# Kernel tuning notes

Measured on AMD Instinct MI355X. Metric: run time of the kernel, lower is better.

Reference implementation:

```python
import jax, jax.numpy as jnp
import numpy as np

N_IN, N_HID, N_OUT = 200, 256, 2
BN_EPS = 1e-5


def _mlp(x, W1, b1, W2, b2):
    # two-layer MLP with ELU activations (dropout prob = 0.0 -> omitted)
    h = jax.nn.elu(x @ W1 + b1)
    return jax.nn.elu(h @ W2 + b2)


def _batch_norm(x, gamma, beta):
    # torch BatchNorm1d in training mode over flattened (B*E) rows, biased variance
    m = x.mean(axis=(0, 1))
    v = x.var(axis=(0, 1))
    return (x - m) * jax.lax.rsqrt(v + BN_EPS) * gamma + beta


def setup_inputs() -> dict:
    key = jax.random.key(0)
    ks = jax.random.split(key, 12)
    B, N, T, D = 32, 100, 50, 4
    inputs = jax.random.normal(ks[0], (B, N, T, D), dtype=jnp.float32)
    # one-hot receiver/sender matrices over all N*(N-1) ordered off-diagonal pairs
    idx = np.array([(i, j) for i in range(N) for j in range(N) if i != j])
    eye = np.eye(N, dtype=np.float32)
    rel_rec = jnp.asarray(eye[idx[:, 0]])   # [E, N]
    rel_send = jnp.asarray(eye[idx[:, 1]])  # [E, N]

    def lin(k, fi, fo):  # xavier_normal weight
        std = float(np.sqrt(2.0 / (fi + fo)))
        return jax.random.normal(k, (fi, fo), dtype=jnp.float32) * std

    b = lambda n: jnp.full((n,), 0.1, dtype=jnp.float32)
    return dict(
        inputs=inputs, rel_rec=rel_rec, rel_send=rel_send,
        mlp1_W1=lin(ks[1], N_IN, N_HID), mlp1_b1=b(N_HID),
        mlp1_W2=lin(ks[2], N_HID, N_HID), mlp1_b2=b(N_HID),
        mlp2_W1=lin(ks[3], 2 * N_HID, N_HID), mlp2_b1=b(N_HID),
        mlp2_W2=lin(ks[4], N_HID, N_HID), mlp2_b2=b(N_HID),
        mlp3_W1=lin(ks[5], N_HID, N_HID), mlp3_b1=b(N_HID),
        mlp3_W2=lin(ks[6], N_HID, N_HID), mlp3_b2=b(N_HID),
        mlp4_W1=lin(ks[7], 3 * N_HID, N_HID), mlp4_b1=b(N_HID),
        mlp4_W2=lin(ks[8], N_HID, N_HID), mlp4_b2=b(N_HID),
        mlp4_bn_gamma=jnp.ones((N_HID,), jnp.float32),
        mlp4_bn_beta=jnp.zeros((N_HID,), jnp.float32),
        fc_W=lin(ks[9], N_HID, N_OUT), fc_b=b(N_OUT),
    )


def reference(inputs, rel_rec, rel_send,
              mlp1_W1, mlp1_b1, mlp1_W2, mlp1_b2,
              mlp2_W1, mlp2_b1, mlp2_W2, mlp2_b2,
              mlp3_W1, mlp3_b1, mlp3_W2, mlp3_b2,
              mlp4_W1, mlp4_b1, mlp4_W2, mlp4_b2,
              mlp4_bn_gamma, mlp4_bn_beta, fc_W, fc_b):
    B, N = inputs.shape[0], inputs.shape[1]
    x = inputs.reshape(B, N, -1)                       # [B, N, T*D]
    x = _mlp(x, mlp1_W1, mlp1_b1, mlp1_W2, mlp1_b2)     # [B, N, H]

    def node2edge(h):
        recv = jnp.einsum('en,bnh->beh', rel_rec, h)
        send = jnp.einsum('en,bnh->beh', rel_send, h)
        return jnp.concatenate([send, recv], axis=2)    # [B, E, 2H]

    x = node2edge(x)
    x = _mlp(x, mlp2_W1, mlp2_b1, mlp2_W2, mlp2_b2)     # [B, E, H]
    x_skip = x
    # factor=True branch
    incoming = jnp.einsum('en,beh->bnh', rel_rec, x) / x.shape[1]  # edge2node, /N per code
    x = _mlp(incoming, mlp3_W1, mlp3_b1, mlp3_W2, mlp3_b2)
    x = node2edge(x)                                    # [B, E, 2H]
    x = jnp.concatenate([x, x_skip], axis=2)            # [B, E, 3H]
    x = _mlp(x, mlp4_W1, mlp4_b1, mlp4_W2, mlp4_b2)
    x = _batch_norm(x, mlp4_bn_gamma, mlp4_bn_beta)
    return x @ fc_W + fc_b                              # [B, E, n_out]
```

## Files before the change

kernel.cpp:

```cpp
#include <hip/hip_runtime.h>
#include <math.h>


typedef unsigned short ushort_t;
typedef __bf16 bf16x8 __attribute__((ext_vector_type(8)));
typedef float  f32x4  __attribute__((ext_vector_type(4)));

#define E_EDGES 9900
#define NNODE   100
#define HID     256
#define M_BIG   316800
#define M_SMALL 3200
#define NBLK2   (M_BIG / 128)

__device__ __forceinline__ float bf2f(ushort_t u) {
    union { unsigned int i; float f; } v; v.i = ((unsigned int)u) << 16; return v.f;
}
__device__ __forceinline__ ushort_t f2bf(float f) {
    union { float f; unsigned int i; } v; v.f = f;
    return (ushort_t)((v.i + 0x7fffu + ((v.i >> 16) & 1u)) >> 16);
}
__device__ __forceinline__ float elu_f(float x) {
    return x > 0.f ? x : (__expf(x) - 1.f);
}

__global__ __launch_bounds__(256)
void wcvt_all(const float* __restrict__ s0, const float* __restrict__ s1,
              const float* __restrict__ s2, const float* __restrict__ s3,
              const float* __restrict__ s4, const float* __restrict__ s5,
              const float* __restrict__ s6, const float* __restrict__ s7,
              ushort_t* d0, ushort_t* d1, ushort_t* d2, ushort_t* d3,
              ushort_t* d4, ushort_t* d5, ushort_t* d6, ushort_t* d7)
{
    int bid = blockIdx.x;
    const float* S; ushort_t* D; int Kd, Kr, t;
    if      (bid < 16)  { S = s0; D = d0; Kd = 256; Kr = 200; t = bid; }
    else if (bid < 32)  { S = s1; D = d1; Kd = 256; Kr = 256; t = bid - 16; }
    else if (bid < 64)  { S = s2; D = d2; Kd = 512; Kr = 512; t = bid - 32; }
    else if (bid < 80)  { S = s3; D = d3; Kd = 256; Kr = 256; t = bid - 64; }
    else if (bid < 96)  { S = s4; D = d4; Kd = 256; Kr = 256; t = bid - 80; }
    else if (bid < 112) { S = s5; D = d5; Kd = 256; Kr = 256; t = bid - 96; }
    else if (bid < 160) { S = s6; D = d6; Kd = 768; Kr = 768; t = bid - 112; }
    else                { S = s7; D = d7; Kd = 256; Kr = 256; t = bid - 160; }
    int k0 = (t >> 2) * 64, c0 = (t & 3) * 64;
    __shared__ float Sh[64][65];
    int tid = threadIdx.x;
    #pragma unroll
    for (int i = 0; i < 16; ++i) {
        int idx = tid + i * 256;
        int kk = idx >> 6, cc = idx & 63;
        Sh[kk][cc] = (k0 + kk < Kr) ? S[(size_t)(k0 + kk) * 256 + c0 + cc] : 0.f;
    }
    __syncthreads();
    int col = tid & 63;
    int kb  = (tid >> 6) * 16;
    ushort_t* dst = D + (size_t)(c0 + col) * Kd + k0 + kb;
    #pragma unroll
    for (int jj = 0; jj < 4; ++jj) {
        ushort4 u;
        u.x = f2bf(Sh[kb + 4 * jj + 0][col]);
        u.y = f2bf(Sh[kb + 4 * jj + 1][col]);
        u.z = f2bf(Sh[kb + 4 * jj + 2][col]);
        u.w = f2bf(Sh[kb + 4 * jj + 3][col]);
        *(ushort4*)(dst + 4 * jj) = u;
    }
}

__device__ __forceinline__ void gemm32(const ushort_t S[32][264],
                                       const ushort_t* __restrict__ WT,
                                       int wstr, int kcn,
                                       int w, int ln15, int klane,
                                       f32x4 acc[2][4])
{
    #pragma unroll
    for (int r = 0; r < 2; ++r)
        #pragma unroll
        for (int c = 0; c < 4; ++c)
            acc[r][c][0] = acc[r][c][1] = acc[r][c][2] = acc[r][c][3] = 0.f;
    int wch[4];
    #pragma unroll
    for (int c = 0; c < 4; ++c) wch[c] = (w * 64 + 16 * c + ln15) * wstr;
    bf16x8 wf0[4];
    #pragma unroll
    for (int c = 0; c < 4; ++c)
        wf0[c] = *(const bf16x8*)(WT + wch[c] + klane);
    for (int kc = 0; kc < kcn; ++kc) {
        bf16x8 wf1[4];
        if (kc + 1 < kcn) {
            #pragma unroll
            for (int c = 0; c < 4; ++c)
                wf1[c] = *(const bf16x8*)(WT + wch[c] + (kc + 1) * 32 + klane);
        }
        bf16x8 af[2];
        #pragma unroll
        for (int r = 0; r < 2; ++r)
            af[r] = *(const bf16x8*)&S[16 * r + ln15][kc * 32 + klane];
        #pragma unroll
        for (int r = 0; r < 2; ++r)
            #pragma unroll
            for (int c = 0; c < 4; ++c)
                acc[r][c] = __builtin_amdgcn_mfma_f32_16x16x32_bf16(wf0[c], af[r], acc[r][c], 0, 0, 0);
        #pragma unroll
        for (int c = 0; c < 4; ++c) wf0[c] = wf1[c];
    }
}

__device__ __forceinline__ void park32(ushort_t D[32][264], f32x4 acc[2][4],
                                       const float* __restrict__ bias,
                                       int act, int w, int ln15, int q)
{
    #pragma unroll
    for (int c = 0; c < 4; ++c) {
        float4 bv = bias ? *(const float4*)&bias[w * 64 + 16 * c + 4 * q]
                         : make_float4(0.f, 0.f, 0.f, 0.f);
        #pragma unroll
        for (int r = 0; r < 2; ++r) {
            float o0 = acc[r][c][0] + bv.x;
            float o1 = acc[r][c][1] + bv.y;
            float o2 = acc[r][c][2] + bv.z;
            float o3 = acc[r][c][3] + bv.w;
            if (act) { o0 = elu_f(o0); o1 = elu_f(o1); o2 = elu_f(o2); o3 = elu_f(o3); }
            ushort4 u;
            u.x = f2bf(o0); u.y = f2bf(o1); u.z = f2bf(o2); u.w = f2bf(o3);
            *(ushort4*)&D[16 * r + ln15][w * 64 + 16 * c + 4 * q] = u;
        }
    }
}

__global__ __launch_bounds__(256, 4)
void mlp_pq(const float* __restrict__ Xf, int Kreal, int kcN, float xscale,
            const ushort_t* __restrict__ W1T, const float* __restrict__ b1,
            const ushort_t* __restrict__ W2T, const float* __restrict__ b2,
            const ushort_t* __restrict__ WPT, int wsPQ,
            const float* __restrict__ bP, ushort_t* __restrict__ Pout,
            const ushort_t* __restrict__ WQT, ushort_t* __restrict__ Qout)
{
    __shared__ ushort_t Abuf[32][264];
    __shared__ ushort_t Bbuf[32][264];
    const int tid = threadIdx.x;
    const int w = tid >> 6;
    const int l = tid & 63;
    const int ln15 = l & 15;
    const int q = l >> 4;
    const int klane = 8 * q;
    const int Rbase = blockIdx.x * 32;

    {
        int row = tid >> 3, seg = tid & 7;
        if (seg < kcN) {
            ushort_t tmp[32];
            const float* src = Xf + (size_t)(Rbase + row) * Kreal + seg * 32;
            #pragma unroll
            for (int u = 0; u < 32; ++u)
                tmp[u] = (seg * 32 + u < Kreal) ? f2bf(src[u] * xscale) : (ushort_t)0;
            #pragma unroll
            for (int u = 0; u < 4; ++u)
                *(uint4*)&Abuf[row][seg * 32 + u * 8] = *(uint4*)&tmp[u * 8];
        }
    }
    __syncthreads();

    f32x4 acc[2][4];
    gemm32(Abuf, W1T, 256, kcN, w, ln15, klane, acc);
    park32(Bbuf, acc, b1, 1, w, ln15, q);
    __syncthreads();
    gemm32(Bbuf, W2T, 256, 8, w, ln15, klane, acc);
    park32(Abuf, acc, b2, 1, w, ln15, q);
    __syncthreads();
    gemm32(Abuf, WPT, wsPQ, 8, w, ln15, klane, acc);
    park32(Bbuf, acc, bP, 0, w, ln15, q);
    __syncthreads();
    f32x4 acq[2][4];
    gemm32(Abuf, WQT, wsPQ, 8, w, ln15, klane, acq);
    #pragma unroll
    for (int m = 0; m < 4; ++m) {
        int ch = tid + m * 256;
        int row = ch >> 5;
        int o = (ch & 31) * 8;
        *(uint4*)&Pout[(size_t)(Rbase + row) * 256 + o] = *(const uint4*)&Bbuf[row][o];
    }
    __syncthreads();
    park32(Bbuf, acq, nullptr, 0, w, ln15, q);
    __syncthreads();
    #pragma unroll
    for (int m = 0; m < 4; ++m) {
        int ch = tid + m * 256;
        int row = ch >> 5;
        int o = (ch & 31) * 8;
        *(uint4*)&Qout[(size_t)(Rbase + row) * 256 + o] = *(const uint4*)&Bbuf[row][o];
    }
}

__global__ __launch_bounds__(256, 2)
void edge_mlp2(const ushort_t* __restrict__ Pb, const ushort_t* __restrict__ Qb,
               const ushort_t* __restrict__ W2T,
               const float* __restrict__ b2,
               ushort_t* __restrict__ Y, float* __restrict__ aux)
{
    __shared__ ushort_t As[128][264];
    const int tid = threadIdx.x;
    const int w = tid >> 6;
    const int l = tid & 63;
    const int ln15 = l & 15;
    const int q = l >> 4;
    const int klane = 8 * q;
    const int Rbase = blockIdx.x * 128;

    for (int h = 0; h < 2; ++h) {
        int row = (tid >> 2) + 64 * h;
        int R = Rbase + row;
        int b = R / E_EDGES;
        int e = R - b * E_EDGES;
        int i = e / 99;
        int k = e - 99 * i;
        int j = k + (k >= i ? 1 : 0);
        const ushort_t* prow = Pb + (size_t)(b * NNODE + j) * HID;
        const ushort_t* qrow = Qb + (size_t)(b * NNODE + i) * HID;
        int off = (tid & 3) * 8;
        uint4 pv[8], qv[8];
        #pragma unroll
        for (int u = 0; u < 8; ++u) {
            int o = off + u * 32;
            pv[u] = *(const uint4*)(prow + o);
            qv[u] = *(const uint4*)(qrow + o);
        }
        #pragma unroll
        for (int u = 0; u < 8; ++u) {
            int o = off + u * 32;
            union { uint4 v; ushort_t s[8]; } pu, qu, hu;
            pu.v = pv[u]; qu.v = qv[u];
            #pragma unroll
            for (int x = 0; x < 8; ++x)
                hu.s[x] = f2bf(elu_f(bf2f(pu.s[x]) + bf2f(qu.s[x])));
            *(uint4*)&As[row][o] = hu.v;
        }
    }
    __syncthreads();

    f32x4 acc[8][4];
    #pragma unroll
    for (int r = 0; r < 8; ++r)
        #pragma unroll
        for (int c = 0; c < 4; ++c)
            acc[r][c][0] = acc[r][c][1] = acc[r][c][2] = acc[r][c][3] = 0.f;
    int wch[4];
    #pragma unroll
    for (int c = 0; c < 4; ++c) wch[c] = (w * 64 + 16 * c + ln15) * 256;
    {
        bf16x8 wf0[4];
        #pragma unroll
        for (int c = 0; c < 4; ++c)
            wf0[c] = *(const bf16x8*)(W2T + wch[c] + klane);
        #pragma unroll
        for (int kc = 0; kc < 8; ++kc) {
            bf16x8 wf1[4];
            if (kc < 7) {
                #pragma unroll
                for (int c = 0; c < 4; ++c)
                    wf1[c] = *(const bf16x8*)(W2T + wch[c] + (kc + 1) * 32 + klane);
            }
            bf16x8 af[8];
            #pragma unroll
            for (int r = 0; r < 8; ++r)
                af[r] = *(const bf16x8*)&As[16 * r + ln15][kc * 32 + klane];
            #pragma unroll
            for (int r = 0; r < 8; ++r)
                #pragma unroll
                for (int c = 0; c < 4; ++c)
                    acc[r][c] = __builtin_amdgcn_mfma_f32_16x16x32_bf16(wf0[c], af[r], acc[r][c], 0, 0, 0);
            #pragma unroll
            for (int c = 0; c < 4; ++c) wf0[c] = wf1[c];
        }
    }
    __syncthreads();

    #pragma unroll
    for (int c = 0; c < 4; ++c) {
        float4 bv = *(const float4*)&b2[w * 64 + 16 * c + 4 * q];
        #pragma unroll
        for (int r = 0; r < 8; ++r) {
            ushort4 u;
            u.x = f2bf(elu_f(acc[r][c][0] + bv.x));
            u.y = f2bf(elu_f(acc[r][c][1] + bv.y));
            u.z = f2bf(elu_f(acc[r][c][2] + bv.z));
            u.w = f2bf(elu_f(acc[r][c][3] + bv.w));
            *(ushort4*)&As[16 * r + ln15][w * 64 + 16 * c + 4 * q] = u;
        }
    }
    __syncthreads();

    #pragma unroll
    for (int m = 0; m < 16; ++m) {
        int ch = tid + m * 256;
        int row = ch >> 5;
        int o = (ch & 31) * 8;
        *(uint4*)&Y[((size_t)(Rbase + row)) * 256 + o] = *(const uint4*)&As[row][o];
    }

    if (tid < 64) {
        int c4 = tid * 4;
        int bn = Rbase / 99;
        int left = 99 - (Rbase - bn * 99);
        float s[4] = {0.f, 0.f, 0.f, 0.f};
        for (int r = 0; r < 128; ++r) {
            union { ushort4 v; ushort_t e[4]; } u;
            u.v = *(const ushort4*)&As[r][c4];
            #pragma unroll
            for (int g = 0; g < 4; ++g) s[g] += bf2f(u.e[g]);
            if (--left == 0) {
                #pragma unroll
                for (int g = 0; g < 4; ++g) {
                    atomicAdd(&aux[(size_t)bn * 256 + c4 + g], s[g]);
                    s[g] = 0.f;
                }
                ++bn; left = 99;
            }
        }
        #pragma unroll
        for (int g = 0; g < 4; ++g)
            atomicAdd(&aux[(size_t)bn * 256 + c4 + g], s[g]);
    }
}

__global__ __launch_bounds__(256, 2)
void edge_mlp4(const ushort_t* __restrict__ Pb, const ushort_t* __restrict__ Qb,
               const ushort_t* __restrict__ X2,
               const ushort_t* __restrict__ WaT, int wsA,
               const ushort_t* __restrict__ WbT, int wsB,
               const float* __restrict__ b2,
               ushort_t* __restrict__ Y, ushort_t* __restrict__ pstat)
{
    __shared__ ushort_t As[128][264];
    const int tid = threadIdx.x;
    const int w = tid >> 6;
    const int l = tid & 63;
    const int ln15 = l & 15;
    const int q = l >> 4;
    const int klane = 8 * q;
    const int Rbase = blockIdx.x * 128;

    uint4 xv[2][8];
    #pragma unroll
    for (int h = 0; h < 2; ++h) {
        int row = (tid >> 2) + 64 * h;
        const ushort_t* xrow = X2 + (size_t)(Rbase + row) * 256;
        int off = (tid & 3) * 8;
        #pragma unroll
        for (int u = 0; u < 8; ++u) xv[h][u] = *(const uint4*)(xrow + off + u * 32);
    }

    int oP[8], oQ[8];
    #pragma unroll
    for (int r = 0; r < 8; ++r) {
        int R = Rbase + 16 * r + ln15;
        int b = R / E_EDGES;
        int e = R - b * E_EDGES;
        int i = e / 99;
        int k = e - 99 * i;
        int j = k + (k >= i ? 1 : 0);
        oP[r] = (b * NNODE + j) * HID;
        oQ[r] = (b * NNODE + i) * HID;
    }
    ushort4 pv0[8], qv0[8];
    {
        int ch0 = w * 64 + 4 * q;
        #pragma unroll
        for (int r = 0; r < 8; ++r) {
            pv0[r] = *(const ushort4*)(Pb + oP[r] + ch0);
            qv0[r] = *(const ushort4*)(Qb + oQ[r] + ch0);
        }
    }

    #pragma unroll
    for (int h = 0; h < 2; ++h) {
        int row = (tid >> 2) + 64 * h;
        int off = (tid & 3) * 8;
        #pragma unroll
        for (int u = 0; u < 8; ++u) *(uint4*)&As[row][off + u * 32] = xv[h][u];
    }
    __syncthreads();

    f32x4 acc[8][4];
    int wchA[4], wchB[4];
    #pragma unroll
    for (int c = 0; c < 4; ++c) {
        wchA[c] = (w * 64 + 16 * c + ln15) * wsA;
        wchB[c] = (w * 64 + 16 * c + ln15) * wsB;
    }

    #pragma unroll
    for (int r = 0; r < 8; ++r)
        #pragma unroll
        for (int c = 0; c < 4; ++c)
            acc[r][c][0] = acc[r][c][1] = acc[r][c][2] = acc[r][c][3] = 0.f;
    {
        bf16x8 wf0[4];
        #pragma unroll
        for (int c = 0; c < 4; ++c)
            wf0[c] = *(const bf16x8*)(WaT + wchA[c] + klane);
        #pragma unroll
        for (int kc = 0; kc < 8; ++kc) {
            bf16x8 wf1[4];
            if (kc < 7) {
                #pragma unroll
                for (int c = 0; c < 4; ++c)
                    wf1[c] = *(const bf16x8*)(WaT + wchA[c] + (kc + 1) * 32 + klane);
            }
            bf16x8 af[8];
            #pragma unroll
            for (int r = 0; r < 8; ++r)
                af[r] = *(const bf16x8*)&As[16 * r + ln15][kc * 32 + klane];
            #pragma unroll
            for (int r = 0; r < 8; ++r)
                #pragma unroll
                for (int c = 0; c < 4; ++c)
                    acc[r][c] = __builtin_amdgcn_mfma_f32_16x16x32_bf16(wf0[c], af[r], acc[r][c], 0, 0, 0);
            #pragma unroll
            for (int c = 0; c < 4; ++c) wf0[c] = wf1[c];
        }
    }
    __syncthreads();

    #pragma unroll
    for (int c = 0; c < 4; ++c) {
        ushort4 pv1[8], qv1[8];
        if (c < 3) {
            int chn = w * 64 + 16 * (c + 1) + 4 * q;
            #pragma unroll
            for (int r = 0; r < 8; ++r) {
                pv1[r] = *(const ushort4*)(Pb + oP[r] + chn);
                qv1[r] = *(const ushort4*)(Qb + oQ[r] + chn);
            }
        }
        int ch = w * 64 + 16 * c + 4 * q;
        #pragma unroll
        for (int r = 0; r < 8; ++r) {
            union { ushort4 v; ushort_t s[4]; } pu, qu;
            pu.v = pv0[r]; qu.v = qv0[r];
            ushort4 u;
            u.x = f2bf(elu_f(acc[r][c][0] + bf2f(pu.s[0]) + bf2f(qu.s[0])));
            u.y = f2bf(elu_f(acc[r][c][1] + bf2f(pu.s[1]) + bf2f(qu.s[1])));
            u.z = f2bf(elu_f(acc[r][c][2] + bf2f(pu.s[2]) + bf2f(qu.s[2])));
            u.w = f2bf(elu_f(acc[r][c][3] + bf2f(pu.s[3]) + bf2f(qu.s[3])));
            *(ushort4*)&As[16 * r + ln15][ch] = u;
        }
        #pragma unroll
        for (int r = 0; r < 8; ++r) { pv0[r] = pv1[r]; qv0[r] = qv1[r]; }
    }
    __syncthreads();

    #pragma unroll
    for (int r = 0; r < 8; ++r)
        #pragma unroll
        for (int c = 0; c < 4; ++c)
            acc[r][c][0] = acc[r][c][1] = acc[r][c][2] = acc[r][c][3] = 0.f;
    {
        bf16x8 wf0[4];
        #pragma unroll
        for (int c = 0; c < 4; ++c)
            wf0[c] = *(const bf16x8*)(WbT + wchB[c] + klane);
        #pragma unroll
        for (int kc = 0; kc < 8; ++kc) {
            bf16x8 wf1[4];
            if (kc < 7) {
                #pragma unroll
                for (int c = 0; c < 4; ++c)
                    wf1[c] = *(const bf16x8*)(WbT + wchB[c] + (kc + 1) * 32 + klane);
            }
            bf16x8 af[8];
            #pragma unroll
            for (int r = 0; r < 8; ++r)
                af[r] = *(const bf16x8*)&As[16 * r + ln15][kc * 32 + klane];
            #pragma unroll
            for (int r = 0; r < 8; ++r)
                #pragma unroll
                for (int c = 0; c < 4; ++c)
                    acc[r][c] = __builtin_amdgcn_mfma_f32_16x16x32_bf16(wf0[c], af[r], acc[r][c], 0, 0, 0);
            #pragma unroll
            for (int c = 0; c < 4; ++c) wf0[c] = wf1[c];
        }
    }
    __syncthreads();

    #pragma unroll
    for (int c = 0; c < 4; ++c) {
        float4 bv = *(const float4*)&b2[w * 64 + 16 * c + 4 * q];
        #pragma unroll
        for (int r = 0; r < 8; ++r) {
            ushort4 u;
            u.x = f2bf(elu_f(acc[r][c][0] + bv.x));
            u.y = f2bf(elu_f(acc[r][c][1] + bv.y));
            u.z = f2bf(elu_f(acc[r][c][2] + bv.z));
            u.w = f2bf(elu_f(acc[r][c][3] + bv.w));
            *(ushort4*)&As[16 * r + ln15][w * 64 + 16 * c + 4 * q] = u;
        }
    }
    __syncthreads();

    #pragma unroll
    for (int m = 0; m < 16; ++m) {
        int ch = tid + m * 256;
        int row = ch >> 5;
        int o = (ch & 31) * 8;
        *(uint4*)&Y[((size_t)(Rbase + row)) * 256 + o] = *(const uint4*)&As[row][o];
    }

    if (tid < 64) {
        int c4 = tid * 4;
        float s[4] = {0.f, 0.f, 0.f, 0.f};
        float qq[4] = {0.f, 0.f, 0.f, 0.f};
        for (int r = 0; r < 128; ++r) {
            union { ushort4 v; ushort_t e[4]; } u;
            u.v = *(const ushort4*)&As[r][c4];
            #pragma unroll
            for (int g = 0; g < 4; ++g) {
                float v = bf2f(u.e[g]);
                s[g] += v;
                qq[g] = fmaf(v, v, qq[g]);
            }
        }
        size_t base = (size_t)blockIdx.x * 512;
        ushort4 us, uq;
        us.x = f2bf(s[0]);  us.y = f2bf(s[1]);  us.z = f2bf(s[2]);  us.w = f2bf(s[3]);
        uq.x = f2bf(qq[0]); uq.y = f2bf(qq[1]); uq.z = f2bf(qq[2]); uq.w = f2bf(qq[3]);
        *(ushort4*)&pstat[base + c4]       = us;
        *(ushort4*)&pstat[base + 256 + c4] = uq;
    }
}

__global__ __launch_bounds__(256)
void reduce_stats(const ushort_t* __restrict__ pstat, float* __restrict__ stats)
{
    int c = threadIdx.x;
    float s = 0.f, q = 0.f;
    for (int b = blockIdx.x; b < NBLK2; b += 64) {
        size_t base = (size_t)b * 512;
        s += bf2f(pstat[base + c]);
        q += bf2f(pstat[base + 256 + c]);
    }
    atomicAdd(&stats[c], s);
    atomicAdd(&stats[256 + c], q);
}

__global__ __launch_bounds__(256)
void fold_kernel(const float* __restrict__ stats,
                 const float* __restrict__ gamma, const float* __restrict__ beta,
                 const float* __restrict__ fcW, const float* __restrict__ fcb,
                 float* __restrict__ fold)
{
    __shared__ float red0[256], red1[256];
    int c = threadIdx.x;
    float mean  = stats[c] * (1.f / M_BIG);
    float var   = stats[256 + c] * (1.f / M_BIG) - mean * mean;
    float inv   = rsqrtf(var + 1e-5f);
    float scale = inv * gamma[c];
    float sh    = beta[c] - mean * scale;
    float w0 = fcW[c * 2 + 0], w1 = fcW[c * 2 + 1];
    fold[c * 2 + 0] = scale * w0;
    fold[c * 2 + 1] = scale * w1;
    red0[c] = sh * w0;
    red1[c] = sh * w1;
    __syncthreads();
    for (int off = 128; off > 0; off >>= 1) {
        if (c < off) { red0[c] += red0[c + off]; red1[c] += red1[c + off]; }
        __syncthreads();
    }
    if (c == 0) {
        fold[512] = red0[0] + fcb[0];
        fold[513] = red1[0] + fcb[1];
    }
}

__global__ __launch_bounds__(256)
void final_kernel(const ushort_t* __restrict__ x4, const float* __restrict__ fold,
                  float* __restrict__ out)
{
    int tid  = threadIdx.x;
    int l32  = tid & 31;
    int g    = tid >> 5;
    int R = blockIdx.x * 8 + g;
    int c0 = l32 * 8;
    union { uint4 qv; ushort_t s[8]; } u;
    u.qv = *(const uint4*)(x4 + (size_t)R * 256 + c0);
    float a0 = 0.f, a1 = 0.f;
    #pragma unroll
    for (int j = 0; j < 8; ++j) {
        float v = bf2f(u.s[j]);
        a0 = fmaf(v, fold[(c0 + j) * 2 + 0], a0);
        a1 = fmaf(v, fold[(c0 + j) * 2 + 1], a1);
    }
    #pragma unroll
    for (int off = 16; off > 0; off >>= 1) {
        a0 += __shfl_down(a0, off);
        a1 += __shfl_down(a1, off);
    }
    if (l32 == 0) {
        out[(size_t)R * 2 + 0] = a0 + fold[512];
        out[(size_t)R * 2 + 1] = a1 + fold[513];
    }
}

extern "C" void kernel_launch(void* const* d_in, const int* in_sizes, int n_in,
                              void* d_out, int out_size, void* d_ws, size_t ws_size,
                              hipStream_t stream)
{
    (void)in_sizes; (void)n_in; (void)out_size; (void)ws_size;

    const float* inputs = (const float*)d_in[0];
    const float* m1W1 = (const float*)d_in[3];
    const float* m1b1 = (const float*)d_in[4];
    const float* m1W2 = (const float*)d_in[5];
    const float* m1b2 = (const float*)d_in[6];
    const float* m2W1 = (const float*)d_in[7];
    const float* m2b1 = (const float*)d_in[8];
    const float* m2W2 = (const float*)d_in[9];
    const float* m2b2 = (const float*)d_in[10];
    const float* m3W1 = (const float*)d_in[11];
    const float* m3b1 = (const float*)d_in[12];
    const float* m3W2 = (const float*)d_in[13];
    const float* m3b2 = (const float*)d_in[14];
    const float* m4W1 = (const float*)d_in[15];
    const float* m4b1 = (const float*)d_in[16];
    const float* m4W2 = (const float*)d_in[17];
    const float* m4b2 = (const float*)d_in[18];
    const float* gamma = (const float*)d_in[19];
    const float* beta  = (const float*)d_in[20];
    const float* fcW   = (const float*)d_in[21];
    const float* fcb   = (const float*)d_in[22];
    float* out = (float*)d_out;

    char* ws = (char*)d_ws;
    const size_t BIGB = (size_t)M_BIG * 256 * 2;
    const size_t HB   = (size_t)M_SMALL * 256 * 2;
    const size_t SM4  = (size_t)M_SMALL * 256 * 4;
    ushort_t* bigX     = (ushort_t*)ws;
    ushort_t* pstat    = (ushort_t*)(ws + BIGB);
    float*    incoming = (float*)(ws + BIGB + 2 * HB);
    ushort_t* Pbuf     = (ushort_t*)(ws + BIGB + 2 * HB + SM4);
    ushort_t* Qbuf     = (ushort_t*)(ws + BIGB + 3 * HB + SM4);
    float*    stats    = (float*)(ws + BIGB + 4 * HB + SM4);
    float*    fold     = stats + 512;
    ushort_t* w1t      = (ushort_t*)(ws + BIGB + 4 * HB + SM4 + 8192);
    ushort_t* w1bt     = w1t  + 256 * 256;
    ushort_t* w2pt     = w1bt + 256 * 256;
    ushort_t* w2t      = w2pt + 256 * 512;
    ushort_t* w3at     = w2t  + 256 * 256;
    ushort_t* w3bt     = w3at + 256 * 256;
    ushort_t* w4pt     = w3bt + 256 * 256;
    ushort_t* w4bt     = w4pt + 256 * 768;

    hipMemsetAsync(stats, 0, 2048, stream);
    hipMemsetAsync(incoming, 0, SM4, stream);

    dim3 blk(256);
    wcvt_all<<<176, blk, 0, stream>>>(m1W1, m1W2, m2W1, m2W2, m3W1, m3W2, m4W1, m4W2,
                                      w1t, w1bt, w2pt, w2t, w3at, w3bt, w4pt, w4bt);
    mlp_pq<<<100, blk, 0, stream>>>(inputs, 200, 7, 1.f,
                                    w1t, m1b1, w1bt, m1b2,
                                    w2pt, 512, m2b1, Pbuf,
                                    w2pt + 256, Qbuf);
    edge_mlp2<<<NBLK2, blk, 0, stream>>>(Pbuf, Qbuf, w2t, m2b2, bigX, incoming);
    mlp_pq<<<100, blk, 0, stream>>>(incoming, 256, 8, 1.f / 9900.f,
                                    w3at, m3b1, w3bt, m3b2,
                                    w4pt, 768, m4b1, Pbuf,
                                    w4pt + 256, Qbuf);
    edge_mlp4<<<NBLK2, blk, 0, stream>>>(Pbuf, Qbuf, bigX,
                                         w4pt + 512, 768, w4bt, 256,
                                         m4b2, bigX, pstat);
    reduce_stats<<<64, blk, 0, stream>>>(pstat, stats);
    fold_kernel<<<1, blk, 0, stream>>>(stats, gamma, beta, fcW, fcb, fold);
    final_kernel<<<M_BIG / 8, blk, 0, stream>>>(bigX, fold, out);
}
```

Measured before the change: 520.1 us.

## Use 512-thread blocks in edge MLP kernels with 32-column warp tiles

The edge_mlp2 and edge_mlp4 kernels move from 256 to 512 threads per block. Each of the eight warps now owns 32 output columns instead of 64, which halves the accumulator registers and allows more waves per CU. The GEMM loop is moved into a shared helper that issues A-fragment loads in two groups of four rows to reduce register pressure. In edge_mlp4 the software prefetch of P/Q rows is removed, trading some latency hiding for lower register use, and each warp now does more LDS reads per MFMA.

Result: faster. 494.5 us (-4.9%).

```diff
diff --git a/kernel.cpp b/kernel.cpp
--- a/kernel.cpp
+++ b/kernel.cpp
@@ -191,7 +191,49 @@
     }
 }
 
-__global__ __launch_bounds__(256, 2)
+__device__ __forceinline__ void gemm128cs(const ushort_t As[128][264],
+                                          const ushort_t* __restrict__ WT,
+                                          int wstr, int w, int ln15, int klane,
+                                          f32x4 acc[8][2])
+{
+    #pragma unroll
+    for (int r = 0; r < 8; ++r)
+        #pragma unroll
+        for (int c = 0; c < 2; ++c)
+            acc[r][c][0] = acc[r][c][1] = acc[r][c][2] = acc[r][c][3] = 0.f;
+    int wch[2];
+    #pragma unroll
+    for (int c = 0; c < 2; ++c) wch[c] = (w * 32 + 16 * c + ln15) * wstr;
+    bf16x8 wf0[2];
+    #pragma unroll
+    for (int c = 0; c < 2; ++c)
+        wf0[c] = *(const bf16x8*)(WT + wch[c] + klane);
+    #pragma unroll
+    for (int kc = 0; kc < 8; ++kc) {
+        bf16x8 wf1[2];
+        if (kc < 7) {
+            #pragma unroll
+            for (int c = 0; c < 2; ++c)
+                wf1[c] = *(const bf16x8*)(WT + wch[c] + (kc + 1) * 32 + klane);
+        }
+        #pragma unroll
+        for (int g = 0; g < 2; ++g) {
+            bf16x8 af[4];
+            #pragma unroll
+            for (int r = 0; r < 4; ++r)
+                af[r] = *(const bf16x8*)&As[16 * (4 * g + r) + ln15][kc * 32 + klane];
+            #pragma unroll
+            for (int r = 0; r < 4; ++r)
+                #pragma unroll
+                for (int c = 0; c < 2; ++c)
+                    acc[4 * g + r][c] = __builtin_amdgcn_mfma_f32_16x16x32_bf16(wf0[c], af[r], acc[4 * g + r][c], 0, 0, 0);
+        }
+        #pragma unroll
+        for (int c = 0; c < 2; ++c) wf0[c] = wf1[c];
+    }
+}
+
+__global__ __launch_bounds__(512, 4)
 void edge_mlp2(const ushort_t* __restrict__ Pb, const ushort_t* __restrict__ Qb,
                const ushort_t* __restrict__ W2T,
                const float* __restrict__ b2,
@@ -206,8 +248,8 @@
     const int klane = 8 * q;
     const int Rbase = blockIdx.x * 128;
 
-    for (int h = 0; h < 2; ++h) {
-        int row = (tid >> 2) + 64 * h;
+    {
+        int row = tid >> 2;
         int R = Rbase + row;
         int b = R / E_EDGES;
         int e = R - b * E_EDGES;
@@ -237,46 +279,13 @@
     }
     __syncthreads();
 
-    f32x4 acc[8][4];
-    #pragma unroll
-    for (int r = 0; r < 8; ++r)
-        #pragma unroll
-        for (int c = 0; c < 4; ++c)
-            acc[r][c][0] = acc[r][c][1] = acc[r][c][2] = acc[r][c][3] = 0.f;
-    int wch[4];
-    #pragma unroll
-    for (int c = 0; c < 4; ++c) wch[c] = (w * 64 + 16 * c + ln15) * 256;
-    {
-        bf16x8 wf0[4];
-        #pragma unroll
-        for (int c = 0; c < 4; ++c)
-            wf0[c] = *(const bf16x8*)(W2T + wch[c] + klane);
-        #pragma unroll
-        for (int kc = 0; kc < 8; ++kc) {
-            bf16x8 wf1[4];
-            if (kc < 7) {
-                #pragma unroll
-                for (int c = 0; c < 4; ++c)
-                    wf1[c] = *(const bf16x8*)(W2T + wch[c] + (kc + 1) * 32 + klane);
-            }
-            bf16x8 af[8];
-            #pragma unroll
-            for (int r = 0; r < 8; ++r)
-                af[r] = *(const bf16x8*)&As[16 * r + ln15][kc * 32 + klane];
-            #pragma unroll
-            for (int r = 0; r < 8; ++r)
-                #pragma unroll
-                for (int c = 0; c < 4; ++c)
-                    acc[r][c] = __builtin_amdgcn_mfma_f32_16x16x32_bf16(wf0[c], af[r], acc[r][c], 0, 0, 0);
-            #pragma unroll
-            for (int c = 0; c < 4; ++c) wf0[c] = wf1[c];
-        }
-    }
-    __syncthreads();
-
-    #pragma unroll
-    for (int c = 0; c < 4; ++c) {
-        float4 bv = *(const float4*)&b2[w * 64 + 16 * c + 4 * q];
+    f32x4 acc[8][2];
+    gemm128cs(As, W2T, 256, w, ln15, klane, acc);
+    __syncthreads();
+
+    #pragma unroll
+    for (int c = 0; c < 2; ++c) {
+        float4 bv = *(const float4*)&b2[w * 32 + 16 * c + 4 * q];
         #pragma unroll
         for (int r = 0; r < 8; ++r) {
             ushort4 u;
@@ -284,14 +293,14 @@
             u.y = f2bf(elu_f(acc[r][c][1] + bv.y));
             u.z = f2bf(elu_f(acc[r][c][2] + bv.z));
             u.w = f2bf(elu_f(acc[r][c][3] + bv.w));
-            *(ushort4*)&As[16 * r + ln15][w * 64 + 16 * c + 4 * q] = u;
-        }
-    }
-    __syncthreads();
-
-    #pragma unroll
-    for (int m = 0; m < 16; ++m) {
-        int ch = tid + m * 256;
+            *(ushort4*)&As[16 * r + ln15][w * 32 + 16 * c + 4 * q] = u;
+        }
+    }
+    __syncthreads();
+
+    #pragma unroll
+    for (int m = 0; m < 8; ++m) {
+        int ch = tid + m * 512;
         int row = ch >> 5;
         int o = (ch & 31) * 8;
         *(uint4*)&Y[((size_t)(Rbase + row)) * 256 + o] = *(const uint4*)&As[row][o];
@@ -322,7 +331,7 @@
     }
 }
 
-__global__ __launch_bounds__(256, 2)
+__global__ __launch_bounds__(512, 4)
 void edge_mlp4(const ushort_t* __restrict__ Pb, const ushort_t* __restrict__ Qb,
                const ushort_t* __restrict__ X2,
                const ushort_t* __restrict__ WaT, int wsA,
@@ -339,14 +348,15 @@
     const int klane = 8 * q;
     const int Rbase = blockIdx.x * 128;
 
-    uint4 xv[2][8];
-    #pragma unroll
-    for (int h = 0; h < 2; ++h) {
-        int row = (tid >> 2) + 64 * h;
+    {
+        int row = tid >> 2;
         const ushort_t* xrow = X2 + (size_t)(Rbase + row) * 256;
         int off = (tid & 3) * 8;
-        #pragma unroll
-        for (int u = 0; u < 8; ++u) xv[h][u] = *(const uint4*)(xrow + off + u * 32);
+        uint4 xv[8];
+        #pragma unroll
+        for (int u = 0; u < 8; ++u) xv[u] = *(const uint4*)(xrow + off + u * 32);
+        #pragma unroll
+        for (int u = 0; u < 8; ++u) *(uint4*)&As[row][off + u * 32] = xv[u];
     }
 
     int oP[8], oQ[8];
@@ -361,82 +371,25 @@
         oP[r] = (b * NNODE + j) * HID;
         oQ[r] = (b * NNODE + i) * HID;
     }
-    ushort4 pv0[8], qv0[8];
-    {
-        int ch0 = w * 64 + 4 * q;
+    __syncthreads();
+
+    f32x4 acc[8][2];
+    gemm128cs(As, WaT, wsA, w, ln15, klane, acc);
+    __syncthreads();
+
+    #pragma unroll
+    for (int c = 0; c < 2; ++c) {
+        int ch = w * 32 + 16 * c + 4 * q;
+        ushort4 pv[8], qv[8];
         #pragma unroll
         for (int r = 0; r < 8; ++r) {
-            pv0[r] = *(const ushort4*)(Pb + oP[r] + ch0);
-            qv0[r] = *(const ushort4*)(Qb + oQ[r] + ch0);
-        }
-    }
-
-    #pragma unroll
-    for (int h = 0; h < 2; ++h) {
-        int row = (tid >> 2) + 64 * h;
-        int off = (tid & 3) * 8;
-        #pragma unroll
-        for (int u = 0; u < 8; ++u) *(uint4*)&As[row][off + u * 32] = xv[h][u];
-    }
-    __syncthreads();
-
-    f32x4 acc[8][4];
-    int wchA[4], wchB[4];
-    #pragma unroll
-    for (int c = 0; c < 4; ++c) {
-        wchA[c] = (w * 64 + 16 * c + ln15) * wsA;
-        wchB[c] = (w * 64 + 16 * c + ln15) * wsB;
-    }
-
-    #pragma unroll
-    for (int r = 0; r < 8; ++r)
-        #pragma unroll
-        for (int c = 0; c < 4; ++c)
-            acc[r][c][0] = acc[r][c][1] = acc[r][c][2] = acc[r][c][3] = 0.f;
-    {
-        bf16x8 wf0[4];
-        #pragma unroll
-        for (int c = 0; c < 4; ++c)
-            wf0[c] = *(const bf16x8*)(WaT + wchA[c] + klane);
-        #pragma unroll
-        for (int kc = 0; kc < 8; ++kc) {
-            bf16x8 wf1[4];
-            if (kc < 7) {
-                #pragma unroll
-                for (int c = 0; c < 4; ++c)
-                    wf1[c] = *(const bf16x8*)(WaT + wchA[c] + (kc + 1) * 32 + klane);
-            }
-            bf16x8 af[8];
-            #pragma unroll
-            for (int r = 0; r < 8; ++r)
-                af[r] = *(const bf16x8*)&As[16 * r + ln15][kc * 32 + klane];
-            #pragma unroll
-            for (int r = 0; r < 8; ++r)
-                #pragma unroll
-                for (int c = 0; c < 4; ++c)
-                    acc[r][c] = __builtin_amdgcn_mfma_f32_16x16x32_bf16(wf0[c], af[r], acc[r][c], 0, 0, 0);
-            #pragma unroll
-            for (int c = 0; c < 4; ++c) wf0[c] = wf1[c];
-        }
-    }
-    __syncthreads();
-
-    #pragma unroll
-    for (int c = 0; c < 4; ++c) {
-        ushort4 pv1[8], qv1[8];
-        if (c < 3) {
-            int chn = w * 64 + 16 * (c + 1) + 4 * q;
-            #pragma unroll
-            for (int r = 0; r < 8; ++r) {
-                pv1[r] = *(const ushort4*)(Pb + oP[r] + chn);
-                qv1[r] = *(const ushort4*)(Qb + oQ[r] + chn);
-            }
-        }
-        int ch = w * 64 + 16 * c + 4 * q;
+            pv[r] = *(const ushort4*)(Pb + oP[r] + ch);
+            qv[r] = *(const ushort4*)(Qb + oQ[r] + ch);
+        }
         #pragma unroll
         for (int r = 0; r < 8; ++r) {
             union { ushort4 v; ushort_t s[4]; } pu, qu;
-            pu.v = pv0[r]; qu.v = qv0[r];
+            pu.v = pv[r]; qu.v = qv[r];
             ushort4 u;
             u.x = f2bf(elu_f(acc[r][c][0] + bf2f(pu.s[0]) + bf2f(qu.s[0])));
             u.y = f2bf(elu_f(acc[r][c][1] + bf2f(pu.s[1]) + bf2f(qu.s[1])));
@@ -444,47 +397,15 @@
             u.w = f2bf(elu_f(acc[r][c][3] + bf2f(pu.s[3]) + bf2f(qu.s[3])));
             *(ushort4*)&As[16 * r + ln15][ch] = u;
         }
-        #pragma unroll
-        for (int r = 0; r < 8; ++r) { pv0[r] = pv1[r]; qv0[r] = qv1[r]; }
-    }
-    __syncthreads();
-
-    #pragma unroll
-    for (int r = 0; r < 8; ++r)
-        #pragma unroll
-        for (int c = 0; c < 4; ++c)
-            acc[r][c][0] = acc[r][c][1] = acc[r][c][2] = acc[r][c][3] = 0.f;
-    {
-        bf16x8 wf0[4];
-        #pragma unroll
-        for (int c = 0; c < 4; ++c)
-            wf0[c] = *(const bf16x8*)(WbT + wchB[c] + klane);
-        #pragma unroll
-        for (int kc = 0; kc < 8; ++kc) {
-            bf16x8 wf1[4];
-            if (kc < 7) {
-                #pragma unroll
-                for (int c = 0; c < 4; ++c)
-                    wf1[c] = *(const bf16x8*)(WbT + wchB[c] + (kc + 1) * 32 + klane);
-            }
-            bf16x8 af[8];
-            #pragma unroll
-            for (int r = 0; r < 8; ++r)
-                af[r] = *(const bf16x8*)&As[16 * r + ln15][kc * 32 + klane];
-            #pragma unroll
-            for (int r = 0; r < 8; ++r)
-                #pragma unroll
-                for (int c = 0; c < 4; ++c)
-                    acc[r][c] = __builtin_amdgcn_mfma_f32_16x16x32_bf16(wf0[c], af[r], acc[r][c], 0, 0, 0);
-            #pragma unroll
-            for (int c = 0; c < 4; ++c) wf0[c] = wf1[c];
-        }
-    }
-    __syncthreads();
-
-    #pragma unroll
-    for (int c = 0; c < 4; ++c) {
-        float4 bv = *(const float4*)&b2[w * 64 + 16 * c + 4 * q];
+    }
+    __syncthreads();
+
+    gemm128cs(As, WbT, wsB, w, ln15, klane, acc);
+    __syncthreads();
+
+    #pragma unroll
+    for (int c = 0; c < 2; ++c) {
+        float4 bv = *(const float4*)&b2[w * 32 + 16 * c + 4 * q];
         #pragma unroll
         for (int r = 0; r < 8; ++r) {
             ushort4 u;
@@ -492,14 +413,14 @@
             u.y = f2bf(elu_f(acc[r][c][1] + bv.y));
             u.z = f2bf(elu_f(acc[r][c][2] + bv.z));
             u.w = f2bf(elu_f(acc[r][c][3] + bv.w));
-            *(ushort4*)&As[16 * r + ln15][w * 64 + 16 * c + 4 * q] = u;
-        }
-    }
-    __syncthreads();
-
-    #pragma unroll
-    for (int m = 0; m < 16; ++m) {
-        int ch = tid + m * 256;
+            *(ushort4*)&As[16 * r + ln15][w * 32 + 16 * c + 4 * q] = u;
+        }
+    }
+    __syncthreads();
+
+    #pragma unroll
+    for (int m = 0; m < 8; ++m) {
+        int ch = tid + m * 512;
         int row = ch >> 5;
         int o = (ch & 31) * 8;
         *(uint4*)&Y[((size_t)(Rbase + row)) * 256 + o] = *(const uint4*)&As[row][o];
@@ -653,20 +574,21 @@
     hipMemsetAsync(incoming, 0, SM4, stream);
 
     dim3 blk(256);
+    dim3 blk512(512);
     wcvt_all<<<176, blk, 0, stream>>>(m1W1, m1W2, m2W1, m2W2, m3W1, m3W2, m4W1, m4W2,
                                       w1t, w1bt, w2pt, w2t, w3at, w3bt, w4pt, w4bt);
     mlp_pq<<<100, blk, 0, stream>>>(inputs, 200, 7, 1.f,
                                     w1t, m1b1, w1bt, m1b2,
                                     w2pt, 512, m2b1, Pbuf,
                                     w2pt + 256, Qbuf);
-    edge_mlp2<<<NBLK2, blk, 0, stream>>>(Pbuf, Qbuf, w2t, m2b2, bigX, incoming);
+    edge_mlp2<<<NBLK2, blk512, 0, stream>>>(Pbuf, Qbuf, w2t, m2b2, bigX, incoming);
     mlp_pq<<<100, blk, 0, stream>>>(incoming, 256, 8, 1.f / 9900.f,
                                     w3at, m3b1, w3bt, m3b2,
                                     w4pt, 768, m4b1, Pbuf,
                                     w4pt + 256, Qbuf);
-    edge_mlp4<<<NBLK2, blk, 0, stream>>>(Pbuf, Qbuf, bigX,
-                                         w4pt + 512, 768, w4bt, 256,
-                                         m4b2, bigX, pstat);
+    edge_mlp4<<<NBLK2, blk512, 0, stream>>>(Pbuf, Qbuf, bigX,
+                                            w4pt + 512, 768, w4bt, 256,
+                                            m4b2, bigX, pstat);
     reduce_stats<<<64, blk, 0, stream>>>(pstat, stats);
     fold_kernel<<<1, blk, 0, stream>>>(stats, gamma, beta, fcW, fcb, fold);
     final_kernel<<<M_BIG / 8, blk, 0, stream>>>(bigX, fold, out);
```
